# Optimization experiments

Hardware: AMD Instinct MI355X
Metric: run time of the kernel (lower is better)

The kernel has to match this reference:

```python
import jax, jax.numpy as jnp
import numpy as np

N, E = 10000, 320000
IN_D, HID, OUT_D, EIN, KH = 128, 32, 128, 1, 32
BN_EPS = 1e-5  # torch BatchNorm1d default eps


def bn(x, g, b):
    # training-mode batch norm with biased variance (torch normalization semantics)
    m = jnp.mean(x, axis=0)
    v = jnp.mean((x - m) ** 2, axis=0)
    return g * (x - m) / jnp.sqrt(v + BN_EPS) + b


def setup_inputs() -> dict:
    key = jax.random.key(0)
    ks = jax.random.split(key, 8)

    def w(k, shape, s=0.05):
        return jax.random.normal(k, shape, dtype=jnp.float32) * s

    return {
        "H": jax.random.normal(ks[0], (N, IN_D), dtype=jnp.float32),
        "edge_attr": jax.random.normal(ks[1], (E, EIN), dtype=jnp.float32),
        "edges": jax.random.randint(ks[2], (2, E), 0, N),
        # linear1: input_dim -> hidden_dim
        "w1": w(ks[3], (HID, IN_D)), "b1": jnp.zeros((HID,), jnp.float32),
        # kernel MLP: edge_input_dim -> kernel_hidden -> (hidden+1)*hidden
        "kw1": w(ks[4], (KH, EIN)), "kb1": jnp.zeros((KH,), jnp.float32),
        "kw2": w(ks[5], ((HID + 1) * HID, KH)), "kb2": jnp.zeros(((HID + 1) * HID,), jnp.float32),
        # linear2: hidden -> output
        "w2": w(ks[6], (OUT_D, HID)), "b2": jnp.zeros((OUT_D,), jnp.float32),
        # batchnorm affine params
        "g_in": jnp.ones((IN_D,), jnp.float32), "beta_in": jnp.zeros((IN_D,), jnp.float32),
        "g_msg": jnp.ones((HID,), jnp.float32), "beta_msg": jnp.zeros((HID,), jnp.float32),
        "g_upd": jnp.ones((HID,), jnp.float32), "beta_upd": jnp.zeros((HID,), jnp.float32),
        "g_out": jnp.ones((OUT_D,), jnp.float32), "beta_out": jnp.zeros((OUT_D,), jnp.float32),
    }


def reference(H, edge_attr, edges, w1, b1, kw1, kb1, kw2, kb2, w2, b2,
              g_in, beta_in, g_msg, beta_msg, g_upd, beta_upd, g_out, beta_out):
    node_out, node_in = edges[0], edges[1]

    Hn = bn(H, g_in, beta_in)                    # input_batch_norm
    layer_input = jax.nn.relu(Hn)                # dropout -> identity (eval)

    # message: gather -> linear1 -> BN -> relu
    msg = layer_input[node_in] @ w1.T + b1       # [E, HID]
    msg = jax.nn.relu(bn(msg, g_msg, beta_msg))

    # edge-conditioned dynamic kernel: [E, HID+1, HID]
    kern = jax.nn.relu(edge_attr @ kw1.T + kb1) @ kw2.T + kb2
    kern = kern.reshape(E, HID + 1, HID)
    # per-edge matvec + per-edge bias row
    msg = jnp.einsum('ejk,ek->ej', kern[:, 1:, :], msg) + kern[:, 0, :]

    # aggregate: scatter_add into nodes
    upd = jax.ops.segment_sum(msg, node_out, num_segments=N)
    upd = jax.nn.relu(bn(upd, g_upd, beta_upd))

    out = upd @ w2.T + b2                        # linear2
    return bn(out, g_out, beta_out)              # output_batch_norm
```

## Files before the change

### kernel.cpp

```cpp
#include <hip/hip_runtime.h>
#include <math.h>

constexpr int N_    = 10000;
constexpr int E_    = 320000;
constexpr int IND   = 128;
constexpr int HID   = 32;
constexpr int OUTD  = 128;
constexpr int NIV   = 33;
constexpr float EPS = 1e-5f;

constexpr size_t OFF_SUMH   = 0;
constexpr size_t OFF_SQH    = 128;
constexpr size_t OFF_SUMP   = 256;
constexpr size_t OFF_SQP    = 288;
constexpr size_t OFF_SUMU   = 320;
constexpr size_t OFF_SQU    = 352;
constexpr size_t OFF_SUMO   = 384;
constexpr size_t OFF_SQO    = 512;
constexpr size_t OFF_OCC    = 640;
constexpr size_t OFF_DEGIN  = 704;
constexpr size_t OFF_DEGOUT = 10704;
constexpr size_t ZERO_CNT   = 20704;
constexpr size_t OFF_STARTS = 20740;
constexpr size_t OFF_CUR    = 30744;
constexpr size_t OFF_C1     = 40744;
constexpr size_t OFF_C0     = 75592;
constexpr size_t OFF_P      = 110440;
constexpr size_t OFF_UPD    = 430440;
constexpr size_t OFF_AEN    = 750440;

__device__ inline int compute_bps(const float* kw1, const float* kb1, float* bp) {
    int m = 0;
    for (int k = 0; k < 32; ++k) {
        float w = kw1[k];
        if (w != 0.f) bp[m++] = -kb1[k] / w;
    }
    for (int a = 1; a < m; ++a) {
        float v = bp[a]; int b = a - 1;
        while (b >= 0 && bp[b] > v) { bp[b+1] = bp[b]; --b; }
        bp[b+1] = v;
    }
    return m;
}

__global__ __launch_bounds__(256)
void k_A(const float* __restrict__ H,
         const float* __restrict__ ea, const int* __restrict__ edges,
         const float* __restrict__ kw1, const float* __restrict__ kb1,
         const float* __restrict__ kw2, const float* __restrict__ kb2,
         float* __restrict__ ws) {
    __shared__ float sel1[32], sel0[32];
    __shared__ float shS[256], shQ[256];
    __shared__ int locc[NIV];
    __shared__ float bps[32];
    int* wsi = (int*)ws;
    int t = threadIdx.x;
    int bid = blockIdx.x;

    if (bid < 33) {
        int i = bid;
        if (t == 0) {
            float bp[32];
            int m = compute_bps(kw1, kb1, bp);
            float arep;
            if (m == 0 || i > m) arep = 0.f;
            else if (i == 0)     arep = bp[0]   - (1.f + 0.5f*fabsf(bp[0]));
            else if (i == m)     arep = bp[m-1] + (1.f + 0.5f*fabsf(bp[m-1]));
            else                 arep = (bp[i-1] < bp[i]) ? 0.5f*(bp[i-1] + bp[i]) : bp[i-1];
            for (int k = 0; k < 32; ++k) {
                bool s = (arep * kw1[k] + kb1[k]) > 0.f;
                sel1[k] = s ? kw1[k] : 0.f;
                sel0[k] = s ? kb1[k] : 0.f;
            }
        }
        __syncthreads();
        for (int r = t; r < 1056; r += 256) {
            float a1 = 0.f, a0 = 0.f;
            for (int k = 0; k < 32; ++k) {
                float w = kw2[r*32 + k];
                a1 += w * sel1[k];
                a0 += w * sel0[k];
            }
            ws[OFF_C1 + (size_t)i*1056 + r] = a1;
            ws[OFF_C0 + (size_t)i*1056 + r] = a0 + kb2[r];
        }
    } else if (bid < 161) {
        int b2 = bid - 33;
        int col = t & 127, half = t >> 7;
        float s = 0.f, q = 0.f;
        for (int r = b2*2 + half; r < N_; r += 128*2) {
            float x = H[(size_t)r*IND + col];
            s += x; q += x*x;
        }
        shS[t] = s; shQ[t] = q;
        __syncthreads();
        if (t < 128) {
            atomicAdd(&ws[OFF_SUMH + t], shS[t] + shS[t+128]);
            atomicAdd(&ws[OFF_SQH  + t], shQ[t] + shQ[t+128]);
        }
    } else {
        int b2 = bid - 161;
        if (t < NIV) locc[t] = 0;
        if (t == 0) {
            float bp[32];
            int m = compute_bps(kw1, kb1, bp);
            for (int k = 0; k < 32; ++k) bps[k] = (k < m) ? bp[k] : 3.0e38f;
        }
        __syncthreads();
        for (int e = b2*256 + t; e < E_; e += 313*256) {
            float a = ea[e];
            int cnt = 0;
            #pragma unroll
            for (int k = 0; k < 32; ++k) cnt += (bps[k] < a) ? 1 : 0;
            atomicAdd(&locc[cnt], 1);
            atomicAdd(&wsi[OFF_DEGIN  + edges[E_ + e]], 1);
            atomicAdd(&wsi[OFF_DEGOUT + edges[e]],      1);
        }
        __syncthreads();
        if (t < NIV && locc[t] > 0) atomicAdd(&wsi[OFF_OCC + t], locc[t]);
    }
}

__global__ __launch_bounds__(256)
void k_B(const float* __restrict__ H, const float* __restrict__ w1,
         const float* __restrict__ b1, const float* __restrict__ g_in,
         const float* __restrict__ beta_in, float* __restrict__ ws) {
    __shared__ float w1L[32*129];
    __shared__ float xl[8][128];
    __shared__ int part[256];
    int* wsi = (int*)ws;
    int t = threadIdx.x;

    if (blockIdx.x == 0) {
        int base = t * 40;
        int loc[40];
        int s = 0;
        for (int i = 0; i < 40; ++i) {
            int idx = base + i;
            int v = (idx < N_) ? wsi[OFF_DEGOUT + idx] : 0;
            loc[i] = s; s += v;
        }
        part[t] = s;
        __syncthreads();
        for (int off = 1; off < 256; off <<= 1) {
            int add = (t >= off) ? part[t - off] : 0;
            __syncthreads();
            part[t] += add;
            __syncthreads();
        }
        int pre = (t > 0) ? part[t-1] : 0;
        for (int i = 0; i < 40; ++i) {
            int idx = base + i;
            if (idx <= N_) {
                int v = pre + loc[i];
                wsi[OFF_STARTS + idx] = v;
                if (idx < N_) wsi[OFF_CUR + idx] = v;
            }
        }
        return;
    }

    int g = t >> 5, j = t & 31;
    for (int idx = t; idx < 4096; idx += 256)
        w1L[(idx >> 7)*129 + (idx & 127)] = w1[idx];

    int n = (blockIdx.x - 1)*8 + g;
    float4 h4 = ((const float4*)(H + (size_t)n*IND))[j];
    float4 m4 = ((const float4*)(ws + OFF_SUMH))[j];
    float4 q4 = ((const float4*)(ws + OFF_SQH))[j];
    float4 gg = ((const float4*)g_in)[j];
    float4 bb = ((const float4*)beta_in)[j];
    float4 xv;
    {
        float* hp = (float*)&h4; float* mp = (float*)&m4; float* qp = (float*)&q4;
        float* gp = (float*)&gg; float* bp = (float*)&bb; float* xp = (float*)&xv;
        for (int i = 0; i < 4; ++i) {
            float mean = mp[i] * (1.f/N_);
            float var  = qp[i] * (1.f/N_) - mean*mean;
            float istd = 1.f / sqrtf(var + EPS);
            float gc = gp[i]*istd, bc = bp[i] - mean*gc;
            xp[i] = fmaxf(fmaf(gc, hp[i], bc), 0.f);
        }
    }
    ((float4*)&xl[g][0])[j] = xv;
    __syncthreads();
    float p = b1[j];
    const float* wr = &w1L[j*129];
    const float* xr = &xl[g][0];
    #pragma unroll 8
    for (int k = 0; k < 128; ++k) p = fmaf(wr[k], xr[k], p);
    ws[OFF_P + (size_t)n*HID + j] = p;
}

__global__ __launch_bounds__(256)
void k_C(const float* __restrict__ ea, const int* __restrict__ edges,
         const float* __restrict__ kw1, const float* __restrict__ kb1,
         float* __restrict__ ws) {
    __shared__ float shS[256], shQ[256];
    __shared__ float bps[32];
    int* wsi = (int*)ws;
    int t = threadIdx.x;
    if (blockIdx.x < 313) {
        if (t == 0) {
            float bp[32];
            int m = compute_bps(kw1, kb1, bp);
            for (int k = 0; k < 32; ++k) bps[k] = (k < m) ? bp[k] : 3.0e38f;
        }
        __syncthreads();
        float2* aen = (float2*)(ws + OFF_AEN);
        int b2 = blockIdx.x;
        for (int e = b2*256 + t; e < E_; e += 313*256) {
            int   nout = edges[e];
            int   nin  = edges[E_ + e];
            float a    = ea[e];
            int iv = 0;
            #pragma unroll
            for (int k = 0; k < 32; ++k) iv += (bps[k] < a) ? 1 : 0;
            int pos = atomicAdd(&wsi[OFF_CUR + nout], 1);
            float2 rec; rec.x = a; rec.y = __int_as_float(nin | (iv << 16));
            aen[pos] = rec;
        }
    } else {
        int b2 = blockIdx.x - 313;
        int j = t & 31, cp = t >> 5;
        float s = 0.f, q = 0.f;
        for (int n = b2*8 + cp; n < N_; n += 64*8) {
            float w = (float)wsi[OFF_DEGIN + n];
            float p = ws[OFF_P + (size_t)n*HID + j];
            s += w*p; q += w*p*p;
        }
        shS[t] = s; shQ[t] = q;
        __syncthreads();
        if (t < 32) {
            float S = 0.f, Qq = 0.f;
            for (int c = 0; c < 8; ++c) { S += shS[t + 32*c]; Qq += shQ[t + 32*c]; }
            atomicAdd(&ws[OFF_SUMP + t], S);
            atomicAdd(&ws[OFF_SQP  + t], Qq);
        }
    }
}

__global__ __launch_bounds__(256)
void k_D(const float* __restrict__ g_msg, const float* __restrict__ beta_msg,
         float* __restrict__ ws) {
    __shared__ float A[4][32*33];
    __shared__ float Bv[4][32];
    __shared__ float zl[8][4][32];
    __shared__ float shS[256], shQ[256];
    __shared__ int s_slot0, s_slot1;
    int* wsi = (int*)ws;
    int t = threadIdx.x, g = t >> 5, j = t & 31;

    if (t == 0) {
        int a0 = -1, a1 = -1;
        for (int i = 0; i < NIV; ++i)
            if (wsi[OFF_OCC + i] > 0) { if (a0 < 0) a0 = i; else if (a1 < 0) a1 = i; }
        s_slot0 = a0; s_slot1 = a1;
    }
    __syncthreads();
    int s0 = s_slot0, s1 = s_slot1;

    for (int idx = t; idx < 1024; idx += 256) {
        int jj = idx >> 5, kk = idx & 31;
        A[0][jj*33+kk] = (s0 >= 0) ? ws[OFF_C1 + (size_t)s0*1056 + 32 + idx] : 0.f;
        A[1][jj*33+kk] = (s0 >= 0) ? ws[OFF_C0 + (size_t)s0*1056 + 32 + idx] : 0.f;
        A[2][jj*33+kk] = (s1 >= 0) ? ws[OFF_C1 + (size_t)s1*1056 + 32 + idx] : 0.f;
        A[3][jj*33+kk] = (s1 >= 0) ? ws[OFF_C0 + (size_t)s1*1056 + 32 + idx] : 0.f;
    }
    if (t < 32) {
        Bv[0][t] = (s0 >= 0) ? ws[OFF_C1 + (size_t)s0*1056 + t] : 0.f;
        Bv[1][t] = (s0 >= 0) ? ws[OFF_C0 + (size_t)s0*1056 + t] : 0.f;
        Bv[2][t] = (s1 >= 0) ? ws[OFF_C1 + (size_t)s1*1056 + t] : 0.f;
        Bv[3][t] = (s1 >= 0) ? ws[OFF_C0 + (size_t)s1*1056 + t] : 0.f;
    }
    float mP = ws[OFF_SUMP + j] * (1.f/E_);
    float vP = ws[OFF_SQP  + j] * (1.f/E_) - mP*mP;
    float istd = 1.f / sqrtf(vP + EPS);
    float gc = g_msg[j]*istd, bc = beta_msg[j] - mP*gc;
    __syncthreads();

    int n = blockIdx.x*8 + g;
    int st = wsi[OFF_STARTS + n], en = wsi[OFF_STARTS + n + 1];
    float za0 = 0.f, zb0 = 0.f, za1 = 0.f, zb1 = 0.f;
    float suma0 = 0.f, suma1 = 0.f, c0f = 0.f, c1f = 0.f, rfall = 0.f;
    const float2* aen = (const float2*)(ws + OFF_AEN);

    for (int base = st; base < en; base += 32) {
        int cnt = en - base; if (cnt > 32) cnt = 32;
        float a_j = 0.f; int meta_j = 0;
        if (j < cnt) {
            float2 r = aen[base + j];
            a_j = r.x; meta_j = __float_as_int(r.y);
        }
        for (int k = 0; k < cnt; k += 4) {
            float pv[4], aa[4]; int ivv[4]; bool val[4];
            #pragma unroll
            for (int u = 0; u < 4; ++u) {
                int kk = (k + u) & 31;
                aa[u]  = __shfl(a_j, kk, 32);
                int mt = __shfl(meta_j, kk, 32);
                val[u] = (k + u) < cnt;
                int nin = mt & 0xFFFF; ivv[u] = mt >> 16;
                pv[u] = ws[OFF_P + (size_t)nin*HID + j];
            }
            #pragma unroll
            for (int u = 0; u < 4; ++u) {
                if (!val[u]) continue;
                float q = fmaxf(fmaf(gc, pv[u], bc), 0.f);
                float a = aa[u]; int iv = ivv[u];
                if (iv == s0)      { za0 = fmaf(a, q, za0); zb0 += q; suma0 += a; c0f += 1.f; }
                else if (iv == s1) { za1 = fmaf(a, q, za1); zb1 += q; suma1 += a; c1f += 1.f; }
                else {
                    const float* C1r = ws + OFF_C1 + (size_t)iv*1056;
                    const float* C0r = ws + OFF_C0 + (size_t)iv*1056;
                    float d1 = 0.f, d0 = 0.f;
                    for (int k2 = 0; k2 < 32; ++k2) {
                        float qk = __shfl(q, k2, 32);
                        d1 += C1r[32 + j*32 + k2] * qk;
                        d0 += C0r[32 + j*32 + k2] * qk;
                    }
                    rfall += a*(d1 + C1r[j]) + (d0 + C0r[j]);
                }
            }
        }
    }
    zl[g][0][j] = za0; zl[g][1][j] = zb0; zl[g][2][j] = za1; zl[g][3][j] = zb1;
    __syncthreads();

    float acc = rfall;
    if (s0 >= 0) acc += suma0*Bv[0][j] + c0f*Bv[1][j];
    if (s1 >= 0) acc += suma1*Bv[2][j] + c1f*Bv[3][j];
    const float* z0 = zl[g][0]; const float* z1 = zl[g][1];
    const float* z2 = zl[g][2]; const float* z3 = zl[g][3];
    #pragma unroll 4
    for (int k = 0; k < 32; ++k) {
        acc += A[0][j*33+k]*z0[k] + A[1][j*33+k]*z1[k]
             + A[2][j*33+k]*z2[k] + A[3][j*33+k]*z3[k];
    }
    ws[OFF_UPD + (size_t)n*HID + j] = acc;

    shS[t] = acc; shQ[t] = acc*acc;
    __syncthreads();
    if (t < 32) {
        float S = 0.f, Qq = 0.f;
        for (int c = 0; c < 8; ++c) { S += shS[t + 32*c]; Qq += shQ[t + 32*c]; }
        atomicAdd(&ws[OFF_SUMU + t], S);
        atomicAdd(&ws[OFF_SQU  + t], Qq);
    }
}

__global__ __launch_bounds__(256)
void k_F(const float* __restrict__ w2, const float* __restrict__ b2,
         const float* __restrict__ g_upd, const float* __restrict__ beta_upd,
         float* __restrict__ ws, float* __restrict__ out) {
    __shared__ float U[2][HID];
    __shared__ float shS[256], shQ[256];
    int t = threadIdx.x, nh = t >> 7, o = t & 127;
    float gc = 0.f, bc = 0.f;
    if (o < 32) {
        float m = ws[OFF_SUMU + o]*(1.f/N_);
        float v = ws[OFF_SQU  + o]*(1.f/N_) - m*m;
        float istd = 1.f/sqrtf(v + EPS);
        gc = g_upd[o]*istd; bc = beta_upd[o] - m*gc;
    }
    float w2r[32];
    for (int k = 0; k < 32; ++k) w2r[k] = w2[o*32 + k];
    float bo = b2[o];
    float sO = 0.f, qO = 0.f;
    for (int base = blockIdx.x*2; base < N_; base += gridDim.x*2) {
        int n = base + nh;
        if (o < 32) {
            float u = ws[OFF_UPD + (size_t)n*HID + o];
            U[nh][o] = fmaxf(fmaf(gc, u, bc), 0.f);
        }
        __syncthreads();
        float v = bo;
        for (int k = 0; k < 32; ++k) v = fmaf(w2r[k], U[nh][k], v);
        out[(size_t)n*OUTD + o] = v;
        sO += v; qO += v*v;
        __syncthreads();
    }
    shS[t] = sO; shQ[t] = qO;
    __syncthreads();
    if (t < 128) {
        atomicAdd(&ws[OFF_SUMO + t], shS[t] + shS[t+128]);
        atomicAdd(&ws[OFF_SQO  + t], shQ[t] + shQ[t+128]);
    }
}

__global__ __launch_bounds__(256)
void k_G(const float* __restrict__ g_out, const float* __restrict__ beta_out,
         const float* __restrict__ ws, float* __restrict__ out) {
    int g = blockIdx.x*blockDim.x + threadIdx.x;
    if (g >= N_*OUTD) return;
    int o = g & 127;
    float m = ws[OFF_SUMO + o]*(1.f/N_);
    float v = ws[OFF_SQO  + o]*(1.f/N_) - m*m;
    float istd = 1.f/sqrtf(v + EPS);
    out[g] = g_out[o]*istd*(out[g] - m) + beta_out[o];
}

extern "C" void kernel_launch(void* const* d_in, const int* in_sizes, int n_in,
                              void* d_out, int out_size, void* d_ws, size_t ws_size,
                              hipStream_t stream) {
    const float* H        = (const float*)d_in[0];
    const float* ea       = (const float*)d_in[1];
    const int*   edges    = (const int*)  d_in[2];
    const float* w1       = (const float*)d_in[3];
    const float* b1       = (const float*)d_in[4];
    const float* kw1      = (const float*)d_in[5];
    const float* kb1      = (const float*)d_in[6];
    const float* kw2      = (const float*)d_in[7];
    const float* kb2      = (const float*)d_in[8];
    const float* w2       = (const float*)d_in[9];
    const float* b2       = (const float*)d_in[10];
    const float* g_in     = (const float*)d_in[11];
    const float* beta_in  = (const float*)d_in[12];
    const float* g_msg    = (const float*)d_in[13];
    const float* beta_msg = (const float*)d_in[14];
    const float* g_upd    = (const float*)d_in[15];
    const float* beta_upd = (const float*)d_in[16];
    const float* g_out    = (const float*)d_in[17];
    const float* beta_out = (const float*)d_in[18];
    float* ws  = (float*)d_ws;
    float* out = (float*)d_out;

    hipMemsetAsync(d_ws, 0, ZERO_CNT*sizeof(float), stream);
    hipLaunchKernelGGL(k_A, dim3(474),  dim3(256), 0, stream, H, ea, edges, kw1, kb1, kw2, kb2, ws);
    hipLaunchKernelGGL(k_B, dim3(1251), dim3(256), 0, stream, H, w1, b1, g_in, beta_in, ws);
    hipLaunchKernelGGL(k_C, dim3(377),  dim3(256), 0, stream, ea, edges, kw1, kb1, ws);
    hipLaunchKernelGGL(k_D, dim3(1250), dim3(256), 0, stream, g_msg, beta_msg, ws);
    hipLaunchKernelGGL(k_F, dim3(250),  dim3(256), 0, stream, w2, b2, g_upd, beta_upd, ws, out);
    hipLaunchKernelGGL(k_G, dim3((N_*OUTD + 255)/256), dim3(256), 0, stream, g_out, beta_out, ws, out);
}
```

Measured before the change: 257.9 us.

## Compute output BN stats analytically via second moments and fuse degree-weighted stats into k_B

```diff
diff --git a/kernel.cpp b/kernel.cpp
--- a/kernel.cpp
+++ b/kernel.cpp
@@ -15,19 +15,19 @@
 constexpr size_t OFF_SQP    = 288;
 constexpr size_t OFF_SUMU   = 320;
 constexpr size_t OFF_SQU    = 352;
-constexpr size_t OFF_SUMO   = 384;
-constexpr size_t OFF_SQO    = 512;
-constexpr size_t OFF_OCC    = 640;
-constexpr size_t OFF_DEGIN  = 704;
-constexpr size_t OFF_DEGOUT = 10704;
-constexpr size_t ZERO_CNT   = 20704;
-constexpr size_t OFF_STARTS = 20740;
-constexpr size_t OFF_CUR    = 30744;
-constexpr size_t OFF_C1     = 40744;
-constexpr size_t OFF_C0     = 75592;
-constexpr size_t OFF_P      = 110440;
-constexpr size_t OFF_UPD    = 430440;
-constexpr size_t OFF_AEN    = 750440;
+constexpr size_t OFF_MU     = 384;
+constexpr size_t OFF_MM     = 416;
+constexpr size_t OFF_OCC    = 1440;
+constexpr size_t OFF_DEGIN  = 1504;
+constexpr size_t OFF_DEGOUT = 11504;
+constexpr size_t ZERO_CNT   = 21504;
+constexpr size_t OFF_STARTS = 21504;
+constexpr size_t OFF_CUR    = 31508;
+constexpr size_t OFF_C1     = 41512;
+constexpr size_t OFF_C0     = 76360;
+constexpr size_t OFF_P      = 111208;
+constexpr size_t OFF_UPD    = 431208;
+constexpr size_t OFF_AEN    = 751208;
 
 __device__ inline int compute_bps(const float* kw1, const float* kb1, float* bp) {
     int m = 0;
@@ -128,6 +128,7 @@
     __shared__ float w1L[32*129];
     __shared__ float xl[8][128];
     __shared__ int part[256];
+    __shared__ float shS[256], shQ[256];
     int* wsi = (int*)ws;
     int t = threadIdx.x;
 
@@ -190,53 +191,43 @@
     #pragma unroll 8
     for (int k = 0; k < 128; ++k) p = fmaf(wr[k], xr[k], p);
     ws[OFF_P + (size_t)n*HID + j] = p;
+
+    float w = (float)wsi[OFF_DEGIN + n];
+    shS[t] = w*p; shQ[t] = w*p*p;
+    __syncthreads();
+    if (t < 32) {
+        float S = 0.f, Qq = 0.f;
+        for (int c = 0; c < 8; ++c) { S += shS[t + 32*c]; Qq += shQ[t + 32*c]; }
+        atomicAdd(&ws[OFF_SUMP + t], S);
+        atomicAdd(&ws[OFF_SQP  + t], Qq);
+    }
 }
 
 __global__ __launch_bounds__(256)
 void k_C(const float* __restrict__ ea, const int* __restrict__ edges,
          const float* __restrict__ kw1, const float* __restrict__ kb1,
          float* __restrict__ ws) {
-    __shared__ float shS[256], shQ[256];
     __shared__ float bps[32];
     int* wsi = (int*)ws;
     int t = threadIdx.x;
-    if (blockIdx.x < 313) {
-        if (t == 0) {
-            float bp[32];
-            int m = compute_bps(kw1, kb1, bp);
-            for (int k = 0; k < 32; ++k) bps[k] = (k < m) ? bp[k] : 3.0e38f;
-        }
-        __syncthreads();
-        float2* aen = (float2*)(ws + OFF_AEN);
-        int b2 = blockIdx.x;
-        for (int e = b2*256 + t; e < E_; e += 313*256) {
-            int   nout = edges[e];
-            int   nin  = edges[E_ + e];
-            float a    = ea[e];
-            int iv = 0;
-            #pragma unroll
-            for (int k = 0; k < 32; ++k) iv += (bps[k] < a) ? 1 : 0;
-            int pos = atomicAdd(&wsi[OFF_CUR + nout], 1);
-            float2 rec; rec.x = a; rec.y = __int_as_float(nin | (iv << 16));
-            aen[pos] = rec;
-        }
-    } else {
-        int b2 = blockIdx.x - 313;
-        int j = t & 31, cp = t >> 5;
-        float s = 0.f, q = 0.f;
-        for (int n = b2*8 + cp; n < N_; n += 64*8) {
-            float w = (float)wsi[OFF_DEGIN + n];
-            float p = ws[OFF_P + (size_t)n*HID + j];
-            s += w*p; q += w*p*p;
-        }
-        shS[t] = s; shQ[t] = q;
-        __syncthreads();
-        if (t < 32) {
-            float S = 0.f, Qq = 0.f;
-            for (int c = 0; c < 8; ++c) { S += shS[t + 32*c]; Qq += shQ[t + 32*c]; }
-            atomicAdd(&ws[OFF_SUMP + t], S);
-            atomicAdd(&ws[OFF_SQP  + t], Qq);
-        }
+    if (t == 0) {
+        float bp[32];
+        int m = compute_bps(kw1, kb1, bp);
+        for (int k = 0; k < 32; ++k) bps[k] = (k < m) ? bp[k] : 3.0e38f;
+    }
+    __syncthreads();
+    float2* aen = (float2*)(ws + OFF_AEN);
+    int b2 = blockIdx.x;
+    for (int e = b2*256 + t; e < E_; e += 313*256) {
+        int   nout = edges[e];
+        int   nin  = edges[E_ + e];
+        float a    = ea[e];
+        int iv = 0;
+        #pragma unroll
+        for (int k = 0; k < 32; ++k) iv += (bps[k] < a) ? 1 : 0;
+        int pos = atomicAdd(&wsi[OFF_CUR + nout], 1);
+        float2 rec; rec.x = a; rec.y = __int_as_float(nin | (iv << 16));
+        aen[pos] = rec;
     }
 }
 
@@ -292,10 +283,10 @@
             float2 r = aen[base + j];
             a_j = r.x; meta_j = __float_as_int(r.y);
         }
-        for (int k = 0; k < cnt; k += 4) {
-            float pv[4], aa[4]; int ivv[4]; bool val[4];
+        for (int k = 0; k < cnt; k += 8) {
+            float pv[8], aa[8]; int ivv[8]; bool val[8];
             #pragma unroll
-            for (int u = 0; u < 4; ++u) {
+            for (int u = 0; u < 8; ++u) {
                 int kk = (k + u) & 31;
                 aa[u]  = __shfl(a_j, kk, 32);
                 int mt = __shfl(meta_j, kk, 32);
@@ -304,22 +295,27 @@
                 pv[u] = ws[OFF_P + (size_t)nin*HID + j];
             }
             #pragma unroll
-            for (int u = 0; u < 4; ++u) {
-                if (!val[u]) continue;
-                float q = fmaxf(fmaf(gc, pv[u], bc), 0.f);
+            for (int u = 0; u < 8; ++u) {
+                float qv = fmaxf(fmaf(gc, pv[u], bc), 0.f);
                 float a = aa[u]; int iv = ivv[u];
-                if (iv == s0)      { za0 = fmaf(a, q, za0); zb0 += q; suma0 += a; c0f += 1.f; }
-                else if (iv == s1) { za1 = fmaf(a, q, za1); zb1 += q; suma1 += a; c1f += 1.f; }
-                else {
+                if (__builtin_expect(val[u] && iv != s0 && iv != s1, 0)) {
                     const float* C1r = ws + OFF_C1 + (size_t)iv*1056;
                     const float* C0r = ws + OFF_C0 + (size_t)iv*1056;
                     float d1 = 0.f, d0 = 0.f;
                     for (int k2 = 0; k2 < 32; ++k2) {
-                        float qk = __shfl(q, k2, 32);
+                        float qk = __shfl(qv, k2, 32);
                         d1 += C1r[32 + j*32 + k2] * qk;
                         d0 += C0r[32 + j*32 + k2] * qk;
                     }
                     rfall += a*(d1 + C1r[j]) + (d0 + C0r[j]);
+                } else {
+                    float w0 = (val[u] && iv == s0) ? 1.f : 0.f;
+                    float w1v = (val[u] && iv == s1) ? 1.f : 0.f;
+                    float w0a = w0 * a, w1a = w1v * a;
+                    za0 = fmaf(w0a, qv, za0); zb0 = fmaf(w0, qv, zb0);
+                    za1 = fmaf(w1a, qv, za1); zb1 = fmaf(w1v, qv, zb1);
+                    suma0 += w0a; c0f += w0;
+                    suma1 += w1a; c1f += w1v;
                 }
             }
         }
@@ -350,54 +346,97 @@
 }
 
 __global__ __launch_bounds__(256)
-void k_F(const float* __restrict__ w2, const float* __restrict__ b2,
+void k_E(const float* __restrict__ g_upd, const float* __restrict__ beta_upd,
+         float* __restrict__ ws) {
+    __shared__ __align__(16) float U[8][36];
+    int t = threadIdx.x;
+    int g = t >> 5, j2 = t & 31;
+    int pj = t >> 3, k4 = (t & 7) * 4;
+
+    float m = ws[OFF_SUMU + j2] * (1.f/N_);
+    float v = ws[OFF_SQU  + j2] * (1.f/N_) - m*m;
+    float istd = 1.f / sqrtf(v + EPS);
+    float gc = g_upd[j2]*istd, bc = beta_upd[j2] - m*gc;
+
+    float accM[4] = {0.f, 0.f, 0.f, 0.f};
+    float accMu = 0.f;
+    for (int c = 0; c < 2; ++c) {
+        int n = (blockIdx.x*2 + c)*8 + g;
+        float uval = fmaxf(fmaf(gc, ws[OFF_UPD + (size_t)n*HID + j2], bc), 0.f);
+        __syncthreads();
+        U[g][j2] = uval;
+        __syncthreads();
+        #pragma unroll
+        for (int nn = 0; nn < 8; ++nn) {
+            float uj = U[nn][pj];
+            float4 uk = *(const float4*)&U[nn][k4];
+            accM[0] = fmaf(uj, uk.x, accM[0]);
+            accM[1] = fmaf(uj, uk.y, accM[1]);
+            accM[2] = fmaf(uj, uk.z, accM[2]);
+            accM[3] = fmaf(uj, uk.w, accM[3]);
+        }
+        if (g == 0) {
+            #pragma unroll
+            for (int nn = 0; nn < 8; ++nn) accMu += U[nn][j2];
+        }
+    }
+    #pragma unroll
+    for (int i = 0; i < 4; ++i)
+        atomicAdd(&ws[OFF_MM + pj*32 + k4 + i], accM[i]);
+    if (g == 0) atomicAdd(&ws[OFF_MU + j2], accMu);
+}
+
+__global__ __launch_bounds__(256)
+void k_G(const float* __restrict__ w2, const float* __restrict__ b2,
          const float* __restrict__ g_upd, const float* __restrict__ beta_upd,
+         const float* __restrict__ g_out, const float* __restrict__ beta_out,
          float* __restrict__ ws, float* __restrict__ out) {
+    __shared__ float Ml[1024];
+    __shared__ float muL[32];
     __shared__ float U[2][HID];
-    __shared__ float shS[256], shQ[256];
     int t = threadIdx.x, nh = t >> 7, o = t & 127;
-    float gc = 0.f, bc = 0.f;
+
+    for (int idx = t; idx < 1024; idx += 256) Ml[idx] = ws[OFF_MM + idx] * (1.f/N_);
+    if (t < 32) muL[t] = ws[OFF_MU + t] * (1.f/N_);
+
+    float gcU = 0.f, bcU = 0.f;
     if (o < 32) {
         float m = ws[OFF_SUMU + o]*(1.f/N_);
         float v = ws[OFF_SQU  + o]*(1.f/N_) - m*m;
         float istd = 1.f/sqrtf(v + EPS);
-        gc = g_upd[o]*istd; bc = beta_upd[o] - m*gc;
+        gcU = g_upd[o]*istd; bcU = beta_upd[o] - m*gcU;
     }
     float w2r[32];
     for (int k = 0; k < 32; ++k) w2r[k] = w2[o*32 + k];
     float bo = b2[o];
-    float sO = 0.f, qO = 0.f;
+    __syncthreads();
+
+    float mo = bo;
+    for (int k = 0; k < 32; ++k) mo = fmaf(w2r[k], muL[k], mo);
+    float Es2 = 0.f;
+    for (int jj = 0; jj < 32; ++jj) {
+        float inner = 0.f;
+        const float* Mr = &Ml[jj*32];
+        #pragma unroll 8
+        for (int k = 0; k < 32; ++k) inner = fmaf(w2r[k], Mr[k], inner);
+        Es2 = fmaf(w2r[jj], inner, Es2);
+    }
+    float varO = Es2 + 2.f*bo*(mo - bo) + bo*bo - mo*mo;
+    float istdO = 1.f / sqrtf(varO + EPS);
+    float gco = g_out[o]*istdO, bco = beta_out[o] - mo*gco;
+
     for (int base = blockIdx.x*2; base < N_; base += gridDim.x*2) {
         int n = base + nh;
         if (o < 32) {
             float u = ws[OFF_UPD + (size_t)n*HID + o];
-            U[nh][o] = fmaxf(fmaf(gc, u, bc), 0.f);
-        }
-        __syncthreads();
-        float v = bo;
-        for (int k = 0; k < 32; ++k) v = fmaf(w2r[k], U[nh][k], v);
-        out[(size_t)n*OUTD + o] = v;
-        sO += v; qO += v*v;
-        __syncthreads();
-    }
-    shS[t] = sO; shQ[t] = qO;
-    __syncthreads();
-    if (t < 128) {
-        atomicAdd(&ws[OFF_SUMO + t], shS[t] + shS[t+128]);
-        atomicAdd(&ws[OFF_SQO  + t], shQ[t] + shQ[t+128]);
-    }
-}
-
-__global__ __launch_bounds__(256)
-void k_G(const float* __restrict__ g_out, const float* __restrict__ beta_out,
-         const float* __restrict__ ws, float* __restrict__ out) {
-    int g = blockIdx.x*blockDim.x + threadIdx.x;
-    if (g >= N_*OUTD) return;
-    int o = g & 127;
-    float m = ws[OFF_SUMO + o]*(1.f/N_);
-    float v = ws[OFF_SQO  + o]*(1.f/N_) - m*m;
-    float istd = 1.f/sqrtf(v + EPS);
-    out[g] = g_out[o]*istd*(out[g] - m) + beta_out[o];
+            U[nh][o] = fmaxf(fmaf(gcU, u, bcU), 0.f);
+        }
+        __syncthreads();
+        float s = bo;
+        for (int k = 0; k < 32; ++k) s = fmaf(w2r[k], U[nh][k], s);
+        out[(size_t)n*OUTD + o] = fmaf(gco, s, bco);
+        __syncthreads();
+    }
 }
 
 extern "C" void kernel_launch(void* const* d_in, const int* in_sizes, int n_in,
@@ -428,8 +467,8 @@
     hipMemsetAsync(d_ws, 0, ZERO_CNT*sizeof(float), stream);
     hipLaunchKernelGGL(k_A, dim3(474),  dim3(256), 0, stream, H, ea, edges, kw1, kb1, kw2, kb2, ws);
     hipLaunchKernelGGL(k_B, dim3(1251), dim3(256), 0, stream, H, w1, b1, g_in, beta_in, ws);
-    hipLaunchKernelGGL(k_C, dim3(377),  dim3(256), 0, stream, ea, edges, kw1, kb1, ws);
+    hipLaunchKernelGGL(k_C, dim3(313),  dim3(256), 0, stream, ea, edges, kw1, kb1, ws);
     hipLaunchKernelGGL(k_D, dim3(1250), dim3(256), 0, stream, g_msg, beta_msg, ws);
-    hipLaunchKernelGGL(k_F, dim3(250),  dim3(256), 0, stream, w2, b2, g_upd, beta_upd, ws, out);
-    hipLaunchKernelGGL(k_G, dim3((N_*OUTD + 255)/256), dim3(256), 0, stream, g_out, beta_out, ws, out);
-}
+    hipLaunchKernelGGL(k_E, dim3(625),  dim3(256), 0, stream, g_upd, beta_upd, ws);
+    hipLaunchKernelGGL(k_G, dim3(250),  dim3(256), 0, stream, w2, b2, g_upd, beta_upd, g_out, beta_out, ws, out);
+}
```

Result: slower. 345.4 us (+33.9%).
